# Optimization experiments

Measured on AMD Instinct MI355X. Metric: run time of the kernel, lower is better.

Reference implementation:

```python
import jax, jax.numpy as jnp
import numpy as np
import math

NUM_BLOCKS, NUM_LAYERS = 3, 10
CLASSES, RES_CH, DIL_CH, SKIP_CH, END_CH = 256, 32, 32, 256, 256
KERNEL = 2
OUTPUT_LENGTH = 32


def _dilation_schedule():
    sched = []
    init_d = 1
    for _ in range(NUM_BLOCKS):
        new_d = 1
        for _ in range(NUM_LAYERS):
            sched.append((new_d, init_d))
            init_d = new_d
            new_d *= 2
    return sched


def dilate(x, dilation, init_dilation):
    # pytorch-wavenet 'dilate': folds time into batch (or back) via reshape.
    if dilation == init_dilation:
        return x
    n, c, l = x.shape
    df = dilation / init_dilation
    new_l = int(math.ceil(l / df) * df)
    if new_l != l:
        x = jnp.pad(x, ((0, 0), (0, 0), (new_l - l, 0)))  # pad_start with zeros
        l = new_l
    l_new = int(round(l * init_dilation / dilation))
    n_new = int(round(n * dilation / init_dilation))
    # (n,c,l) -> (c,l,n) -> (c,l_new,n_new) -> (n_new,c,l_new)
    return x.transpose(1, 2, 0).reshape(c, l_new, n_new).transpose(2, 0, 1)


def conv1(x, w, b):  # 1x1 conv; w: (out,in)
    return jnp.einsum('oc,bcl->bol', w, x) + b[None, :, None]


def conv2(x, w, b):  # kernel-size-2 'valid' conv; w: (out,in,2)
    return (jnp.einsum('oc,bcl->bol', w[:, :, 0], x[:, :, :-1])
            + jnp.einsum('oc,bcl->bol', w[:, :, 1], x[:, :, 1:])
            + b[None, :, None])


def setup_inputs() -> dict:
    key = jax.random.key(0)
    ks = jax.random.split(key, 16)
    L = NUM_BLOCKS * NUM_LAYERS
    f32 = jnp.float32
    s_in = 1.0 / math.sqrt(CLASSES)
    s_res = 1.0 / math.sqrt(RES_CH * KERNEL)
    s_dil = 1.0 / math.sqrt(DIL_CH)
    s_skip = 1.0 / math.sqrt(SKIP_CH)
    return {
        'x': jax.random.normal(ks[0], (16, CLASSES, 4096), f32),
        'causal_w': jax.random.normal(ks[1], (RES_CH, CLASSES), f32) * s_in,
        'causal_b': jnp.zeros((RES_CH,), f32),
        'filt_w': jax.random.normal(ks[2], (L, DIL_CH, RES_CH, KERNEL), f32) * s_res,
        'filt_b': jnp.zeros((L, DIL_CH), f32),
        'gate_w': jax.random.normal(ks[3], (L, DIL_CH, RES_CH, KERNEL), f32) * s_res,
        'gate_b': jnp.zeros((L, DIL_CH), f32),
        'res_w': jax.random.normal(ks[4], (L, RES_CH, DIL_CH), f32) * s_dil,
        'res_b': jnp.zeros((L, RES_CH), f32),
        'skip_w': jax.random.normal(ks[5], (L, SKIP_CH, DIL_CH), f32) * s_dil,
        'skip_b': jnp.zeros((L, SKIP_CH), f32),
        'end1_w': jax.random.normal(ks[6], (END_CH, SKIP_CH), f32) * s_skip,
        'end1_b': jnp.zeros((END_CH,), f32),
        'end2_w': jax.random.normal(ks[7], (CLASSES, END_CH), f32) * (1.0 / math.sqrt(END_CH)),
        'end2_b': jnp.zeros((CLASSES,), f32),
    }


def reference(x, causal_w, causal_b, filt_w, filt_b, gate_w, gate_b,
              res_w, res_b, skip_w, skip_b, end1_w, end1_b, end2_w, end2_b):
    sched = _dilation_schedule()
    cur = conv1(x, causal_w, causal_b)  # (B, RES_CH, L)
    skip = None
    for i, (d, idil) in enumerate(sched):
        residual = dilate(cur, d, idil)
        f = jnp.tanh(conv2(residual, filt_w[i], filt_b[i]))
        g = jax.nn.sigmoid(conv2(residual, gate_w[i], gate_b[i]))
        z = f * g
        s = z if z.shape[2] == 1 else dilate(z, 1, d)
        s = conv1(s, skip_w[i], skip_b[i])
        skip = s if skip is None else s + skip[:, :, -s.shape[2]:]
        cur = conv1(z, res_w[i], res_b[i]) + residual[:, :, KERNEL - 1:]
    out = jax.nn.relu(skip)
    out = jax.nn.relu(conv1(out, end1_w, end1_b))
    out = conv1(out, end2_w, end2_b)
    n, c, _ = out.shape
    out = out[:, :, -OUTPUT_LENGTH:]
    return out.transpose(0, 2, 1).reshape(n * OUTPUT_LENGTH, c)
```

## Files before the change

kernel.cpp:

```cpp
#include <hip/hip_runtime.h>

#define BATCH   16
#define CLASSES 256
#define TLEN    4096
#define RC      32
#define SKIPC   256
#define ENDC    256
#define NLAYERS 30
#define OUT_T   32


__global__ __launch_bounds__(256) void causal_kernel(
    const float* __restrict__ x, const float* __restrict__ w,
    const float* __restrict__ bias, float* __restrict__ h0)
{
    const int NT = 97;
    int b    = blockIdx.x / NT;
    int tile = blockIdx.x % NT;
    int t0   = 995 + tile * 32;

    __shared__ float xs[CLASSES][32];
    __shared__ float wsm[CLASSES][33];

    for (int idx = threadIdx.x; idx < CLASSES * 32; idx += 256) {
        int cc = idx >> 5, j = idx & 31;
        int t = t0 + j;
        xs[cc][j] = (t < TLEN) ? x[((size_t)b * CLASSES + cc) * TLEN + t] : 0.0f;
    }
    for (int idx = threadIdx.x; idx < RC * CLASSES; idx += 256) {
        int c = idx >> 8, cc = idx & 255;
        wsm[cc][c] = w[idx];
    }
    __syncthreads();

    int c  = threadIdx.x & 31;
    int jb = threadIdx.x >> 5;
    float acc0 = 0.f, acc1 = 0.f, acc2 = 0.f, acc3 = 0.f;
    for (int cc = 0; cc < CLASSES; ++cc) {
        float wv = wsm[cc][c];
        const float4* xr = (const float4*)&xs[cc][0];
        float4 xv = xr[jb];
        acc0 += wv * xv.x; acc1 += wv * xv.y;
        acc2 += wv * xv.z; acc3 += wv * xv.w;
    }
    float bb = bias[c];
    float accs[4] = {acc0, acc1, acc2, acc3};
    #pragma unroll
    for (int k = 0; k < 4; ++k) {
        int t = t0 + jb * 4 + k;
        if (t < TLEN) h0[((size_t)b * RC + c) * TLEN + t] = accs[k] + bb;
    }
}

__global__ __launch_bounds__(256) void layer_kernel(
    const float* __restrict__ hin, float* __restrict__ hout,
    float* __restrict__ zb,
    const float* __restrict__ filt_w, const float* __restrict__ filt_b,
    const float* __restrict__ gate_w, const float* __restrict__ gate_b,
    const float* __restrict__ res_w,  const float* __restrict__ res_b,
    int layer, int d, int A1, int nTiles)
{
    int tile = blockIdx.x % nTiles;
    int b    = blockIdx.x / nTiles;
    int t_lo = 4032 - 64 * tile;

    __shared__ float hc[RC][68];
    __shared__ float hp[RC][68];
    __shared__ float zt[RC][68];
    __shared__ float wf0[RC][33], wf1[RC][33];
    __shared__ float wg0[RC][33], wg1[RC][33];
    __shared__ float wrs[RC][33];
    __shared__ float bfs[RC], bgs[RC], brs[RC];

    {
        const float* fw = filt_w + (size_t)layer * RC * RC * 2;
        const float* gw = gate_w + (size_t)layer * RC * RC * 2;
        const float* rw = res_w  + (size_t)layer * RC * RC;
        for (int idx = threadIdx.x; idx < RC * RC; idx += 256) {
            int c = idx >> 5, c2 = idx & 31;
            wf0[c][c2] = fw[idx * 2];  wf1[c][c2] = fw[idx * 2 + 1];
            wg0[c][c2] = gw[idx * 2];  wg1[c][c2] = gw[idx * 2 + 1];
            wrs[c][c2] = rw[idx];
        }
        if (threadIdx.x < RC) {
            bfs[threadIdx.x] = filt_b[layer * RC + threadIdx.x];
            bgs[threadIdx.x] = gate_b[layer * RC + threadIdx.x];
            brs[threadIdx.x] = res_b[layer * RC + threadIdx.x];
        }
    }
    for (int idx = threadIdx.x; idx < RC * 64; idx += 256) {
        int c2 = idx >> 6, tx = idx & 63;
        const float* row = hin + ((size_t)b * RC + c2) * TLEN;
        int t = t_lo + tx;
        hc[c2][tx] = row[t];
        hp[c2][tx] = row[t - d];
    }
    __syncthreads();

    int c  = threadIdx.x & 31;
    int tl = threadIdx.x >> 5;
    float fa[8], ga[8];
    float bfv = bfs[c], bgv = bgs[c];
    #pragma unroll
    for (int k = 0; k < 8; ++k) { fa[k] = bfv; ga[k] = bgv; }

    #pragma unroll 4
    for (int c2 = 0; c2 < RC; ++c2) {
        float w0f = wf0[c][c2], w1f = wf1[c][c2];
        float w0g = wg0[c][c2], w1g = wg1[c][c2];
        const float4* hcr = (const float4*)&hc[c2][0];
        const float4* hpr = (const float4*)&hp[c2][0];
        float4 c0 = hcr[tl * 2], c1 = hcr[tl * 2 + 1];
        float4 p0 = hpr[tl * 2], p1 = hpr[tl * 2 + 1];
        float hcv[8] = {c0.x, c0.y, c0.z, c0.w, c1.x, c1.y, c1.z, c1.w};
        float hpv[8] = {p0.x, p0.y, p0.z, p0.w, p1.x, p1.y, p1.z, p1.w};
        #pragma unroll
        for (int k = 0; k < 8; ++k) {
            fa[k] += w0f * hpv[k] + w1f * hcv[k];
            ga[k] += w0g * hpv[k] + w1g * hcv[k];
        }
    }
    #pragma unroll
    for (int k = 0; k < 8; ++k) {
        float e2 = __expf(2.0f * fa[k]);
        float th = 1.0f - 2.0f / (e2 + 1.0f);
        float sg = 1.0f / (1.0f + __expf(-ga[k]));
        zt[c][tl * 8 + k] = th * sg;
    }
    __syncthreads();

    float ra[8];
    float brv = brs[c];
    #pragma unroll
    for (int k = 0; k < 8; ++k) ra[k] = brv;
    #pragma unroll 4
    for (int c2 = 0; c2 < RC; ++c2) {
        float wv = wrs[c][c2];
        const float4* zr = (const float4*)&zt[c2][0];
        float4 z0 = zr[tl * 2], z1 = zr[tl * 2 + 1];
        float zv[8] = {z0.x, z0.y, z0.z, z0.w, z1.x, z1.y, z1.z, z1.w};
        #pragma unroll
        for (int k = 0; k < 8; ++k) ra[k] += wv * zv[k];
    }
    #pragma unroll
    for (int k = 0; k < 8; ++k) {
        int tx = tl * 8 + k;
        hp[c][tx] = hc[c][tx] + ra[k];
    }
    __syncthreads();

    for (int idx = threadIdx.x; idx < RC * 64; idx += 256) {
        int c2 = idx >> 6, tx = idx & 63;
        int t = t_lo + tx;
        if (t >= A1) hout[((size_t)b * RC + c2) * TLEN + t] = hp[c2][tx];
    }
    if (tile == 0) {
        for (int idx = threadIdx.x; idx < RC * OUT_T; idx += 256) {
            int c2 = idx >> 5, tt = idx & 31;
            zb[(((size_t)layer * BATCH + b) * RC + c2) * OUT_T + tt] = zt[c2][32 + tt];
        }
    }
}

__global__ __launch_bounds__(256) void end_kernel(
    const float* __restrict__ zb,
    const float* __restrict__ skip_w, const float* __restrict__ skip_b,
    const float* __restrict__ e1w, const float* __restrict__ e1b,
    const float* __restrict__ e2w, const float* __restrict__ e2b,
    float* __restrict__ out)
{
    int b  = blockIdx.x >> 5;
    int tt = blockIdx.x & 31;

    __shared__ float zv[NLAYERS * RC];
    __shared__ float sv[SKIPC];
    __shared__ float e1[ENDC];

    for (int idx = threadIdx.x; idx < NLAYERS * RC; idx += 256) {
        int i = idx >> 5, c = idx & 31;
        zv[idx] = zb[(((size_t)i * BATCH + b) * RC + c) * OUT_T + tt];
    }
    __syncthreads();

    int sc = threadIdx.x;
    float acc = 0.0f;
    for (int i = 0; i < NLAYERS; ++i) {
        acc += skip_b[i * SKIPC + sc];
        const float* sw = skip_w + ((size_t)i * SKIPC + sc) * RC;
        #pragma unroll 8
        for (int c2 = 0; c2 < RC; ++c2) acc += sw[c2] * zv[i * RC + c2];
    }
    sv[sc] = fmaxf(acc, 0.0f);
    __syncthreads();

    float a1 = e1b[sc];
    const float* w1 = e1w + (size_t)sc * SKIPC;
    #pragma unroll 8
    for (int k = 0; k < SKIPC; ++k) a1 += w1[k] * sv[k];
    e1[sc] = fmaxf(a1, 0.0f);
    __syncthreads();

    float a2 = e2b[sc];
    const float* w2 = e2w + (size_t)sc * ENDC;
    #pragma unroll 8
    for (int k = 0; k < ENDC; ++k) a2 += w2[k] * e1[k];
    out[(size_t)blockIdx.x * CLASSES + sc] = a2;
}

extern "C" void kernel_launch(void* const* d_in, const int* in_sizes, int n_in,
                              void* d_out, int out_size, void* d_ws, size_t ws_size,
                              hipStream_t stream)
{
    const float* x        = (const float*)d_in[0];
    const float* causal_w = (const float*)d_in[1];
    const float* causal_b = (const float*)d_in[2];
    const float* filt_w   = (const float*)d_in[3];
    const float* filt_b   = (const float*)d_in[4];
    const float* gate_w   = (const float*)d_in[5];
    const float* gate_b   = (const float*)d_in[6];
    const float* res_w    = (const float*)d_in[7];
    const float* res_b    = (const float*)d_in[8];
    const float* skip_w   = (const float*)d_in[9];
    const float* skip_b   = (const float*)d_in[10];
    const float* e1w      = (const float*)d_in[11];
    const float* e1b      = (const float*)d_in[12];
    const float* e2w      = (const float*)d_in[13];
    const float* e2b      = (const float*)d_in[14];

    const size_t HSZ = (size_t)BATCH * RC * TLEN;
    float* hA = (float*)d_ws;
    float* hB = hA + HSZ;
    float* zb = hB + HSZ;

    causal_kernel<<<dim3(BATCH * 97), dim3(256), 0, stream>>>(x, causal_w, causal_b, hA);

    float* bufs[2] = {hA, hB};
    int S = 3069;
    for (int i = 0; i < NLAYERS; ++i) {
        int d = 1 << (i % 10);
        S -= d;
        int A1    = 4064 - S;
        int nOut  = 4096 - A1;
        int nTiles = (nOut + 63) / 64;
        const float* hin = bufs[i & 1];
        float*       ho  = bufs[(i & 1) ^ 1];
        layer_kernel<<<dim3(BATCH * nTiles), dim3(256), 0, stream>>>(
            hin, ho, zb, filt_w, filt_b, gate_w, gate_b, res_w, res_b,
            i, d, A1, nTiles);
    }

    end_kernel<<<dim3(BATCH * OUT_T), dim3(256), 0, stream>>>(
        zb, skip_w, skip_b, e1w, e1b, e2w, e2b, (float*)d_out);
}
```

Measured before the change: 748.6 us.

## Replace per-column end kernel with three tiled GEMM kernels over all outputs

The single end kernel, which ran one block per (batch, time) column and re-read every weight from global memory in each block, is split into three shared-memory tiled GEMMs: skip accumulation, end1 and end2. Each block now handles a 32x32 tile of channels by columns, and the z buffer layout is changed to channel-major so the 512 columns can be batched together. This cuts redundant weight traffic from global memory. In exchange it adds two extra launches and global round trips for the intermediate activations, and each GEMM runs only 128 blocks.

```diff
diff --git a/kernel.cpp b/kernel.cpp
--- a/kernel.cpp
+++ b/kernel.cpp
@@ -8,6 +8,7 @@
 #define ENDC    256
 #define NLAYERS 30
 #define OUT_T   32
+#define NCOL    (BATCH * OUT_T)
 
 
 __global__ __launch_bounds__(256) void causal_kernel(
@@ -157,54 +158,144 @@
     if (tile == 0) {
         for (int idx = threadIdx.x; idx < RC * OUT_T; idx += 256) {
             int c2 = idx >> 5, tt = idx & 31;
-            zb[(((size_t)layer * BATCH + b) * RC + c2) * OUT_T + tt] = zt[c2][32 + tt];
-        }
-    }
-}
-
-__global__ __launch_bounds__(256) void end_kernel(
-    const float* __restrict__ zb,
+            zb[((size_t)layer * RC + c2) * NCOL + b * OUT_T + tt] = zt[c2][32 + tt];
+        }
+    }
+}
+
+__global__ __launch_bounds__(256) void skip_gemm_kernel(
     const float* __restrict__ skip_w, const float* __restrict__ skip_b,
-    const float* __restrict__ e1w, const float* __restrict__ e1b,
-    const float* __restrict__ e2w, const float* __restrict__ e2b,
-    float* __restrict__ out)
-{
-    int b  = blockIdx.x >> 5;
-    int tt = blockIdx.x & 31;
-
-    __shared__ float zv[NLAYERS * RC];
-    __shared__ float sv[SKIPC];
-    __shared__ float e1[ENDC];
-
-    for (int idx = threadIdx.x; idx < NLAYERS * RC; idx += 256) {
-        int i = idx >> 5, c = idx & 31;
-        zv[idx] = zb[(((size_t)i * BATCH + b) * RC + c) * OUT_T + tt];
-    }
-    __syncthreads();
-
-    int sc = threadIdx.x;
-    float acc = 0.0f;
+    const float* __restrict__ zb, float* __restrict__ skipv)
+{
+    int sc0 = blockIdx.x * 32;
+    int n0  = blockIdx.y * 32;
+
+    __shared__ float Ws[32][36];
+    __shared__ float Zs[32][36];
+    __shared__ float sbs[32];
+
+    if (threadIdx.x < 32) {
+        float s = 0.f;
+        #pragma unroll
+        for (int i = 0; i < NLAYERS; ++i) s += skip_b[i * SKIPC + sc0 + threadIdx.x];
+        sbs[threadIdx.x] = s;
+    }
+
+    int g = threadIdx.x >> 5;
+    int n = threadIdx.x & 31;
+    float acc[4] = {0.f, 0.f, 0.f, 0.f};
+
     for (int i = 0; i < NLAYERS; ++i) {
-        acc += skip_b[i * SKIPC + sc];
-        const float* sw = skip_w + ((size_t)i * SKIPC + sc) * RC;
-        #pragma unroll 8
-        for (int c2 = 0; c2 < RC; ++c2) acc += sw[c2] * zv[i * RC + c2];
-    }
-    sv[sc] = fmaxf(acc, 0.0f);
-    __syncthreads();
-
-    float a1 = e1b[sc];
-    const float* w1 = e1w + (size_t)sc * SKIPC;
-    #pragma unroll 8
-    for (int k = 0; k < SKIPC; ++k) a1 += w1[k] * sv[k];
-    e1[sc] = fmaxf(a1, 0.0f);
-    __syncthreads();
-
-    float a2 = e2b[sc];
-    const float* w2 = e2w + (size_t)sc * ENDC;
-    #pragma unroll 8
-    for (int k = 0; k < ENDC; ++k) a2 += w2[k] * e1[k];
-    out[(size_t)blockIdx.x * CLASSES + sc] = a2;
+        __syncthreads();
+        for (int idx = threadIdx.x; idx < 1024; idx += 256) {
+            int r = idx >> 5, cc = idx & 31;
+            Ws[r][cc] = skip_w[((size_t)i * SKIPC + sc0 + r) * RC + cc];
+        }
+        for (int idx = threadIdx.x; idx < 1024; idx += 256) {
+            int cc = idx >> 5, nn = idx & 31;
+            Zs[nn][cc] = zb[((size_t)i * RC + cc) * NCOL + n0 + nn];
+        }
+        __syncthreads();
+        #pragma unroll
+        for (int k4 = 0; k4 < 8; ++k4) {
+            float4 z4 = *(const float4*)&Zs[n][k4 * 4];
+            #pragma unroll
+            for (int q = 0; q < 4; ++q) {
+                float4 w4 = *(const float4*)&Ws[g + 8 * q][k4 * 4];
+                acc[q] += w4.x * z4.x + w4.y * z4.y + w4.z * z4.z + w4.w * z4.w;
+            }
+        }
+    }
+    #pragma unroll
+    for (int q = 0; q < 4; ++q) {
+        int sc = sc0 + g + 8 * q;
+        skipv[(size_t)sc * NCOL + n0 + n] = fmaxf(acc[q] + sbs[g + 8 * q], 0.f);
+    }
+}
+
+__global__ __launch_bounds__(256) void mid_gemm_kernel(
+    const float* __restrict__ A, const float* __restrict__ bias,
+    const float* __restrict__ V, float* __restrict__ O)
+{
+    int sc0 = blockIdx.x * 32;
+    int n0  = blockIdx.y * 32;
+    __shared__ float Ws[32][36];
+    __shared__ float Zs[32][36];
+
+    int g = threadIdx.x >> 5;
+    int n = threadIdx.x & 31;
+    float acc[4] = {0.f, 0.f, 0.f, 0.f};
+
+    for (int k0 = 0; k0 < SKIPC; k0 += 32) {
+        __syncthreads();
+        for (int idx = threadIdx.x; idx < 1024; idx += 256) {
+            int r = idx >> 5, cc = idx & 31;
+            Ws[r][cc] = A[(size_t)(sc0 + r) * SKIPC + k0 + cc];
+        }
+        for (int idx = threadIdx.x; idx < 1024; idx += 256) {
+            int cc = idx >> 5, nn = idx & 31;
+            Zs[nn][cc] = V[(size_t)(k0 + cc) * NCOL + n0 + nn];
+        }
+        __syncthreads();
+        #pragma unroll
+        for (int k4 = 0; k4 < 8; ++k4) {
+            float4 z4 = *(const float4*)&Zs[n][k4 * 4];
+            #pragma unroll
+            for (int q = 0; q < 4; ++q) {
+                float4 w4 = *(const float4*)&Ws[g + 8 * q][k4 * 4];
+                acc[q] += w4.x * z4.x + w4.y * z4.y + w4.z * z4.z + w4.w * z4.w;
+            }
+        }
+    }
+    #pragma unroll
+    for (int q = 0; q < 4; ++q) {
+        int sc = sc0 + g + 8 * q;
+        O[(size_t)sc * NCOL + n0 + n] = fmaxf(acc[q] + bias[sc], 0.f);
+    }
+}
+
+__global__ __launch_bounds__(256) void out_gemm_kernel(
+    const float* __restrict__ A, const float* __restrict__ bias,
+    const float* __restrict__ V, float* __restrict__ O)
+{
+    int sc0 = blockIdx.x * 32;
+    int n0  = blockIdx.y * 32;
+    __shared__ float Ws[32][36];
+    __shared__ float Zs[32][36];
+    __shared__ float Ot[32][33];
+
+    int g = threadIdx.x >> 5;
+    int n = threadIdx.x & 31;
+    float acc[4] = {0.f, 0.f, 0.f, 0.f};
+
+    for (int k0 = 0; k0 < ENDC; k0 += 32) {
+        __syncthreads();
+        for (int idx = threadIdx.x; idx < 1024; idx += 256) {
+            int r = idx >> 5, cc = idx & 31;
+            Ws[r][cc] = A[(size_t)(sc0 + r) * ENDC + k0 + cc];
+        }
+        for (int idx = threadIdx.x; idx < 1024; idx += 256) {
+            int cc = idx >> 5, nn = idx & 31;
+            Zs[nn][cc] = V[(size_t)(k0 + cc) * NCOL + n0 + nn];
+        }
+        __syncthreads();
+        #pragma unroll
+        for (int k4 = 0; k4 < 8; ++k4) {
+            float4 z4 = *(const float4*)&Zs[n][k4 * 4];
+            #pragma unroll
+            for (int q = 0; q < 4; ++q) {
+                float4 w4 = *(const float4*)&Ws[g + 8 * q][k4 * 4];
+                acc[q] += w4.x * z4.x + w4.y * z4.y + w4.z * z4.z + w4.w * z4.w;
+            }
+        }
+    }
+    #pragma unroll
+    for (int q = 0; q < 4; ++q) Ot[n][g + 8 * q] = acc[q] + bias[sc0 + g + 8 * q];
+    __syncthreads();
+    for (int idx = threadIdx.x; idx < 1024; idx += 256) {
+        int r = idx >> 5, cc = idx & 31;
+        O[(size_t)(n0 + r) * CLASSES + sc0 + cc] = Ot[r][cc];
+    }
 }
 
 extern "C" void kernel_launch(void* const* d_in, const int* in_sizes, int n_in,
@@ -228,9 +319,11 @@
     const float* e2b      = (const float*)d_in[14];
 
     const size_t HSZ = (size_t)BATCH * RC * TLEN;
-    float* hA = (float*)d_ws;
-    float* hB = hA + HSZ;
-    float* zb = hB + HSZ;
+    float* hA    = (float*)d_ws;
+    float* hB    = hA + HSZ;
+    float* zb    = hB + HSZ;
+    float* skipv = zb + (size_t)NLAYERS * RC * NCOL;
+    float* e1v   = skipv + (size_t)SKIPC * NCOL;
 
     causal_kernel<<<dim3(BATCH * 97), dim3(256), 0, stream>>>(x, causal_w, causal_b, hA);
 
@@ -239,8 +332,8 @@
     for (int i = 0; i < NLAYERS; ++i) {
         int d = 1 << (i % 10);
         S -= d;
-        int A1    = 4064 - S;
-        int nOut  = 4096 - A1;
+        int A1     = 4064 - S;
+        int nOut   = 4096 - A1;
         int nTiles = (nOut + 63) / 64;
         const float* hin = bufs[i & 1];
         float*       ho  = bufs[(i & 1) ^ 1];
@@ -249,6 +342,7 @@
             i, d, A1, nTiles);
     }
 
-    end_kernel<<<dim3(BATCH * OUT_T), dim3(256), 0, stream>>>(
-        zb, skip_w, skip_b, e1w, e1b, e2w, e2b, (float*)d_out);
-}
+    skip_gemm_kernel<<<dim3(8, 16), dim3(256), 0, stream>>>(skip_w, skip_b, zb, skipv);
+    mid_gemm_kernel <<<dim3(8, 16), dim3(256), 0, stream>>>(e1w, e1b, skipv, e1v);
+    out_gemm_kernel <<<dim3(8, 16), dim3(256), 0, stream>>>(e2w, e2b, e1v, (float*)d_out);
+}
```

New measurement: 802.8 us. 7.2% more time.

## Fuse layer chain and end MLP into one cooperative kernel with per-batch barriers

Applied to the files above, without the earlier changes.

Replaces the 30 per-layer launches and the end kernel with a single cooperative persistent kernel. Each batch element gets a group of 16 blocks that loop over time tiles and synchronise through atomic counters in global memory between layers. The skip, end1 and end2 stages are spread across the 16 blocks of each group, using shared-memory tiling with a reworked zb layout. This removes per-launch overhead and tail idle time, but adds spin-wait barriers, limits the grid to 256 blocks, and reloads weights once per layer in every block.

```diff
diff --git a/kernel.cpp b/kernel.cpp
--- a/kernel.cpp
+++ b/kernel.cpp
@@ -8,7 +8,9 @@
 #define ENDC    256
 #define NLAYERS 30
 #define OUT_T   32
-
+#define NCOL    512
+#define GBLK    16
+#define NBLK    256
 
 __global__ __launch_bounds__(256) void causal_kernel(
     const float* __restrict__ x, const float* __restrict__ w,
@@ -52,159 +54,244 @@
     }
 }
 
-__global__ __launch_bounds__(256) void layer_kernel(
-    const float* __restrict__ hin, float* __restrict__ hout,
-    float* __restrict__ zb,
+__device__ __forceinline__ void grp_barrier(unsigned* ctr)
+{
+    __syncthreads();
+    if (threadIdx.x == 0) {
+        __threadfence();
+        __hip_atomic_fetch_add(ctr, 1u, __ATOMIC_ACQ_REL, __HIP_MEMORY_SCOPE_AGENT);
+        while (__hip_atomic_load(ctr, __ATOMIC_ACQUIRE, __HIP_MEMORY_SCOPE_AGENT) < GBLK) {
+            __builtin_amdgcn_s_sleep(1);
+        }
+        __threadfence();
+    }
+    __syncthreads();
+}
+
+__global__ void __launch_bounds__(256) chain_kernel(
+    float* __restrict__ hA, float* __restrict__ hB,
+    float* __restrict__ zb, float* __restrict__ skipv, float* __restrict__ e1v,
+    unsigned* __restrict__ bar,
     const float* __restrict__ filt_w, const float* __restrict__ filt_b,
     const float* __restrict__ gate_w, const float* __restrict__ gate_b,
     const float* __restrict__ res_w,  const float* __restrict__ res_b,
-    int layer, int d, int A1, int nTiles)
-{
-    int tile = blockIdx.x % nTiles;
-    int b    = blockIdx.x / nTiles;
-    int t_lo = 4032 - 64 * tile;
-
-    __shared__ float hc[RC][68];
-    __shared__ float hp[RC][68];
-    __shared__ float zt[RC][68];
-    __shared__ float wf0[RC][33], wf1[RC][33];
-    __shared__ float wg0[RC][33], wg1[RC][33];
-    __shared__ float wrs[RC][33];
-    __shared__ float bfs[RC], bgs[RC], brs[RC];
-
-    {
-        const float* fw = filt_w + (size_t)layer * RC * RC * 2;
-        const float* gw = gate_w + (size_t)layer * RC * RC * 2;
-        const float* rw = res_w  + (size_t)layer * RC * RC;
-        for (int idx = threadIdx.x; idx < RC * RC; idx += 256) {
-            int c = idx >> 5, c2 = idx & 31;
-            wf0[c][c2] = fw[idx * 2];  wf1[c][c2] = fw[idx * 2 + 1];
-            wg0[c][c2] = gw[idx * 2];  wg1[c][c2] = gw[idx * 2 + 1];
-            wrs[c][c2] = rw[idx];
-        }
-        if (threadIdx.x < RC) {
-            bfs[threadIdx.x] = filt_b[layer * RC + threadIdx.x];
-            bgs[threadIdx.x] = gate_b[layer * RC + threadIdx.x];
-            brs[threadIdx.x] = res_b[layer * RC + threadIdx.x];
-        }
-    }
-    for (int idx = threadIdx.x; idx < RC * 64; idx += 256) {
-        int c2 = idx >> 6, tx = idx & 63;
-        const float* row = hin + ((size_t)b * RC + c2) * TLEN;
-        int t = t_lo + tx;
-        hc[c2][tx] = row[t];
-        hp[c2][tx] = row[t - d];
-    }
-    __syncthreads();
-
-    int c  = threadIdx.x & 31;
-    int tl = threadIdx.x >> 5;
-    float fa[8], ga[8];
-    float bfv = bfs[c], bgv = bgs[c];
-    #pragma unroll
-    for (int k = 0; k < 8; ++k) { fa[k] = bfv; ga[k] = bgv; }
-
-    #pragma unroll 4
-    for (int c2 = 0; c2 < RC; ++c2) {
-        float w0f = wf0[c][c2], w1f = wf1[c][c2];
-        float w0g = wg0[c][c2], w1g = wg1[c][c2];
-        const float4* hcr = (const float4*)&hc[c2][0];
-        const float4* hpr = (const float4*)&hp[c2][0];
-        float4 c0 = hcr[tl * 2], c1 = hcr[tl * 2 + 1];
-        float4 p0 = hpr[tl * 2], p1 = hpr[tl * 2 + 1];
-        float hcv[8] = {c0.x, c0.y, c0.z, c0.w, c1.x, c1.y, c1.z, c1.w};
-        float hpv[8] = {p0.x, p0.y, p0.z, p0.w, p1.x, p1.y, p1.z, p1.w};
-        #pragma unroll
-        for (int k = 0; k < 8; ++k) {
-            fa[k] += w0f * hpv[k] + w1f * hcv[k];
-            ga[k] += w0g * hpv[k] + w1g * hcv[k];
-        }
-    }
-    #pragma unroll
-    for (int k = 0; k < 8; ++k) {
-        float e2 = __expf(2.0f * fa[k]);
-        float th = 1.0f - 2.0f / (e2 + 1.0f);
-        float sg = 1.0f / (1.0f + __expf(-ga[k]));
-        zt[c][tl * 8 + k] = th * sg;
-    }
-    __syncthreads();
-
-    float ra[8];
-    float brv = brs[c];
-    #pragma unroll
-    for (int k = 0; k < 8; ++k) ra[k] = brv;
-    #pragma unroll 4
-    for (int c2 = 0; c2 < RC; ++c2) {
-        float wv = wrs[c][c2];
-        const float4* zr = (const float4*)&zt[c2][0];
-        float4 z0 = zr[tl * 2], z1 = zr[tl * 2 + 1];
-        float zv[8] = {z0.x, z0.y, z0.z, z0.w, z1.x, z1.y, z1.z, z1.w};
-        #pragma unroll
-        for (int k = 0; k < 8; ++k) ra[k] += wv * zv[k];
-    }
-    #pragma unroll
-    for (int k = 0; k < 8; ++k) {
-        int tx = tl * 8 + k;
-        hp[c][tx] = hc[c][tx] + ra[k];
-    }
-    __syncthreads();
-
-    for (int idx = threadIdx.x; idx < RC * 64; idx += 256) {
-        int c2 = idx >> 6, tx = idx & 63;
-        int t = t_lo + tx;
-        if (t >= A1) hout[((size_t)b * RC + c2) * TLEN + t] = hp[c2][tx];
-    }
-    if (tile == 0) {
-        for (int idx = threadIdx.x; idx < RC * OUT_T; idx += 256) {
-            int c2 = idx >> 5, tt = idx & 31;
-            zb[(((size_t)layer * BATCH + b) * RC + c2) * OUT_T + tt] = zt[c2][32 + tt];
-        }
-    }
-}
-
-__global__ __launch_bounds__(256) void end_kernel(
-    const float* __restrict__ zb,
     const float* __restrict__ skip_w, const float* __restrict__ skip_b,
     const float* __restrict__ e1w, const float* __restrict__ e1b,
     const float* __restrict__ e2w, const float* __restrict__ e2b,
     float* __restrict__ out)
 {
-    int b  = blockIdx.x >> 5;
-    int tt = blockIdx.x & 31;
-
-    __shared__ float zv[NLAYERS * RC];
-    __shared__ float sv[SKIPC];
-    __shared__ float e1[ENDC];
-
-    for (int idx = threadIdx.x; idx < NLAYERS * RC; idx += 256) {
-        int i = idx >> 5, c = idx & 31;
-        zv[idx] = zb[(((size_t)i * BATCH + b) * RC + c) * OUT_T + tt];
-    }
-    __syncthreads();
-
-    int sc = threadIdx.x;
-    float acc = 0.0f;
+    const int tid = threadIdx.x;
+    const int grp = blockIdx.x >> 4;
+    const int g   = blockIdx.x & 15;
+    const int b   = grp;
+
+    union __align__(16) Sh {
+        struct {
+            float hc[RC][68], hp[RC][68], zt[RC][68];
+            float wf0[RC][33], wf1[RC][33], wg0[RC][33], wg1[RC][33], wrs[RC][33];
+            float bfs[RC], bgs[RC], brs[RC];
+        } L;
+        struct { float z[320][32]; float w[10][16][32]; } E1;
+        struct { float v[256][32]; float w[16][256]; } E2;
+    };
+    __shared__ Sh sh;
+
+    int S = 3069;
     for (int i = 0; i < NLAYERS; ++i) {
-        acc += skip_b[i * SKIPC + sc];
-        const float* sw = skip_w + ((size_t)i * SKIPC + sc) * RC;
+        int d = 1 << (i % 10);
+        S -= d;
+        int A1 = 4064 - S;
+        int nT = (4096 - A1 + 63) >> 6;
+        const float* hin = (i & 1) ? hB : hA;
+        float*       hout = (i & 1) ? hA : hB;
+
+        if (g < nT) {
+            const float* fw = filt_w + (size_t)i * RC * RC * 2;
+            const float* gw = gate_w + (size_t)i * RC * RC * 2;
+            const float* rw = res_w  + (size_t)i * RC * RC;
+            for (int idx = tid; idx < RC * RC; idx += 256) {
+                int c = idx >> 5, c2 = idx & 31;
+                sh.L.wf0[c][c2] = fw[idx * 2];  sh.L.wf1[c][c2] = fw[idx * 2 + 1];
+                sh.L.wg0[c][c2] = gw[idx * 2];  sh.L.wg1[c][c2] = gw[idx * 2 + 1];
+                sh.L.wrs[c][c2] = rw[idx];
+            }
+            if (tid < RC) {
+                sh.L.bfs[tid] = filt_b[i * RC + tid];
+                sh.L.bgs[tid] = gate_b[i * RC + tid];
+                sh.L.brs[tid] = res_b[i * RC + tid];
+            }
+
+            for (int tile = g; tile < nT; tile += GBLK) {
+                int t_lo = 4032 - (tile << 6);
+                __syncthreads();
+                for (int idx = tid; idx < RC * 64; idx += 256) {
+                    int c2 = idx >> 6, tx = idx & 63;
+                    const float* row = hin + ((size_t)b * RC + c2) * TLEN;
+                    int t = t_lo + tx;
+                    sh.L.hc[c2][tx] = row[t];
+                    sh.L.hp[c2][tx] = row[t - d];
+                }
+                __syncthreads();
+
+                int c  = tid & 31;
+                int tl = tid >> 5;
+                float fa[8], ga[8];
+                float bfv = sh.L.bfs[c], bgv = sh.L.bgs[c];
+                #pragma unroll
+                for (int k = 0; k < 8; ++k) { fa[k] = bfv; ga[k] = bgv; }
+
+                #pragma unroll 4
+                for (int c2 = 0; c2 < RC; ++c2) {
+                    float w0f = sh.L.wf0[c][c2], w1f = sh.L.wf1[c][c2];
+                    float w0g = sh.L.wg0[c][c2], w1g = sh.L.wg1[c][c2];
+                    const float4* hcr = (const float4*)&sh.L.hc[c2][0];
+                    const float4* hpr = (const float4*)&sh.L.hp[c2][0];
+                    float4 c0 = hcr[tl * 2], c1 = hcr[tl * 2 + 1];
+                    float4 p0 = hpr[tl * 2], p1 = hpr[tl * 2 + 1];
+                    float hcv[8] = {c0.x, c0.y, c0.z, c0.w, c1.x, c1.y, c1.z, c1.w};
+                    float hpv[8] = {p0.x, p0.y, p0.z, p0.w, p1.x, p1.y, p1.z, p1.w};
+                    #pragma unroll
+                    for (int k = 0; k < 8; ++k) {
+                        fa[k] += w0f * hpv[k] + w1f * hcv[k];
+                        ga[k] += w0g * hpv[k] + w1g * hcv[k];
+                    }
+                }
+                #pragma unroll
+                for (int k = 0; k < 8; ++k) {
+                    float e2 = __expf(2.0f * fa[k]);
+                    float th = 1.0f - 2.0f / (e2 + 1.0f);
+                    float sg = 1.0f / (1.0f + __expf(-ga[k]));
+                    sh.L.zt[c][tl * 8 + k] = th * sg;
+                }
+                __syncthreads();
+
+                float ra[8];
+                float brv = sh.L.brs[c];
+                #pragma unroll
+                for (int k = 0; k < 8; ++k) ra[k] = brv;
+                #pragma unroll 4
+                for (int c2 = 0; c2 < RC; ++c2) {
+                    float wv = sh.L.wrs[c][c2];
+                    const float4* zr = (const float4*)&sh.L.zt[c2][0];
+                    float4 z0 = zr[tl * 2], z1 = zr[tl * 2 + 1];
+                    float zv[8] = {z0.x, z0.y, z0.z, z0.w, z1.x, z1.y, z1.z, z1.w};
+                    #pragma unroll
+                    for (int k = 0; k < 8; ++k) ra[k] += wv * zv[k];
+                }
+                #pragma unroll
+                for (int k = 0; k < 8; ++k) {
+                    int tx = tl * 8 + k;
+                    sh.L.hp[c][tx] = sh.L.hc[c][tx] + ra[k];
+                }
+                __syncthreads();
+
+                for (int idx = tid; idx < RC * 64; idx += 256) {
+                    int c2 = idx >> 6, tx = idx & 63;
+                    int t = t_lo + tx;
+                    if (t >= A1) hout[((size_t)b * RC + c2) * TLEN + t] = sh.L.hp[c2][tx];
+                }
+                if (tile == 0) {
+                    for (int idx = tid; idx < RC * OUT_T; idx += 256) {
+                        int c2 = idx >> 5, tt = idx & 31;
+                        zb[((size_t)i * RC + c2) * NCOL + b * OUT_T + tt] =
+                            sh.L.zt[c2][32 + tt];
+                    }
+                }
+            }
+        }
+        grp_barrier(bar + i * GBLK + grp);
+    }
+
+    const int n   = tid & 31;
+    const int s8  = tid >> 5;
+    const int sc0 = g * 16;
+
+    {
+        float a0 = 0.f, a1 = 0.f;
+        const float4* zb4 = (const float4*)zb;
+        const float4* sw4 = (const float4*)skip_w;
+        for (int ch = 0; ch < 3; ++ch) {
+            __syncthreads();
+            for (int idx = tid; idx < 320 * 8; idx += 256) {
+                int kk = idx >> 3, k4 = idx & 7;
+                ((float4*)&sh.E1.z[kk][0])[k4] = zb4[(size_t)(ch * 320 + kk) * 128 + b * 8 + k4];
+            }
+            for (int idx = tid; idx < 10 * 16 * 8; idx += 256) {
+                int l = idx >> 7, rem = idx & 127, r = rem >> 3, k4 = rem & 7;
+                ((float4*)&sh.E1.w[l][r][0])[k4] =
+                    sw4[((size_t)(ch * 10 + l) * SKIPC + sc0 + r) * 8 + k4];
+            }
+            __syncthreads();
+            #pragma unroll
+            for (int l = 0; l < 10; ++l) {
+                #pragma unroll
+                for (int k = 0; k < 32; ++k) {
+                    float zv = sh.E1.z[l * 32 + k][n];
+                    a0 += sh.E1.w[l][s8][k]     * zv;
+                    a1 += sh.E1.w[l][s8 + 8][k] * zv;
+                }
+            }
+        }
+        float sb0 = 0.f, sb1 = 0.f;
+        for (int l = 0; l < NLAYERS; ++l) {
+            sb0 += skip_b[l * SKIPC + sc0 + s8];
+            sb1 += skip_b[l * SKIPC + sc0 + s8 + 8];
+        }
+        skipv[((size_t)b * SKIPC + sc0 + s8) * 32 + n]     = fmaxf(a0 + sb0, 0.f);
+        skipv[((size_t)b * SKIPC + sc0 + s8 + 8) * 32 + n] = fmaxf(a1 + sb1, 0.f);
+    }
+    grp_barrier(bar + NLAYERS * GBLK + grp);
+
+    {
+        for (int idx = tid; idx < 256 * 8; idx += 256) {
+            int r = idx >> 3, k4 = idx & 7;
+            ((float4*)&sh.E2.v[r][0])[k4] =
+                ((const float4*)skipv)[((size_t)b * SKIPC + r) * 8 + k4];
+        }
+        for (int idx = tid; idx < 16 * 64; idx += 256) {
+            int r = idx >> 6, k4 = idx & 63;
+            ((float4*)&sh.E2.w[r][0])[k4] = ((const float4*)e1w)[(size_t)(sc0 + r) * 64 + k4];
+        }
+        __syncthreads();
+        float a0 = e1b[sc0 + s8], a1 = e1b[sc0 + s8 + 8];
         #pragma unroll 8
-        for (int c2 = 0; c2 < RC; ++c2) acc += sw[c2] * zv[i * RC + c2];
-    }
-    sv[sc] = fmaxf(acc, 0.0f);
-    __syncthreads();
-
-    float a1 = e1b[sc];
-    const float* w1 = e1w + (size_t)sc * SKIPC;
-    #pragma unroll 8
-    for (int k = 0; k < SKIPC; ++k) a1 += w1[k] * sv[k];
-    e1[sc] = fmaxf(a1, 0.0f);
-    __syncthreads();
-
-    float a2 = e2b[sc];
-    const float* w2 = e2w + (size_t)sc * ENDC;
-    #pragma unroll 8
-    for (int k = 0; k < ENDC; ++k) a2 += w2[k] * e1[k];
-    out[(size_t)blockIdx.x * CLASSES + sc] = a2;
+        for (int k4 = 0; k4 < 64; ++k4) {
+            float4 w0 = ((const float4*)&sh.E2.w[s8][0])[k4];
+            float4 w1 = ((const float4*)&sh.E2.w[s8 + 8][0])[k4];
+            float v0 = sh.E2.v[k4 * 4 + 0][n], v1 = sh.E2.v[k4 * 4 + 1][n];
+            float v2 = sh.E2.v[k4 * 4 + 2][n], v3 = sh.E2.v[k4 * 4 + 3][n];
+            a0 += w0.x * v0 + w0.y * v1 + w0.z * v2 + w0.w * v3;
+            a1 += w1.x * v0 + w1.y * v1 + w1.z * v2 + w1.w * v3;
+        }
+        e1v[((size_t)b * ENDC + sc0 + s8) * 32 + n]     = fmaxf(a0, 0.f);
+        e1v[((size_t)b * ENDC + sc0 + s8 + 8) * 32 + n] = fmaxf(a1, 0.f);
+    }
+    grp_barrier(bar + (NLAYERS + 1) * GBLK + grp);
+
+    {
+        for (int idx = tid; idx < 256 * 8; idx += 256) {
+            int r = idx >> 3, k4 = idx & 7;
+            ((float4*)&sh.E2.v[r][0])[k4] =
+                ((const float4*)e1v)[((size_t)b * ENDC + r) * 8 + k4];
+        }
+        for (int idx = tid; idx < 16 * 64; idx += 256) {
+            int r = idx >> 6, k4 = idx & 63;
+            ((float4*)&sh.E2.w[r][0])[k4] = ((const float4*)e2w)[(size_t)(sc0 + r) * 64 + k4];
+        }
+        __syncthreads();
+        float a0 = e2b[sc0 + s8], a1 = e2b[sc0 + s8 + 8];
+        #pragma unroll 8
+        for (int k4 = 0; k4 < 64; ++k4) {
+            float4 w0 = ((const float4*)&sh.E2.w[s8][0])[k4];
+            float4 w1 = ((const float4*)&sh.E2.w[s8 + 8][0])[k4];
+            float v0 = sh.E2.v[k4 * 4 + 0][n], v1 = sh.E2.v[k4 * 4 + 1][n];
+            float v2 = sh.E2.v[k4 * 4 + 2][n], v3 = sh.E2.v[k4 * 4 + 3][n];
+            a0 += w0.x * v0 + w0.y * v1 + w0.z * v2 + w0.w * v3;
+            a1 += w1.x * v0 + w1.y * v1 + w1.z * v2 + w1.w * v3;
+        }
+        out[(size_t)(b * OUT_T + n) * CLASSES + sc0 + s8]     = a0;
+        out[(size_t)(b * OUT_T + n) * CLASSES + sc0 + s8 + 8] = a1;
+    }
 }
 
 extern "C" void kernel_launch(void* const* d_in, const int* in_sizes, int n_in,
@@ -226,29 +313,26 @@
     const float* e1b      = (const float*)d_in[12];
     const float* e2w      = (const float*)d_in[13];
     const float* e2b      = (const float*)d_in[14];
+    float* outp           = (float*)d_out;
 
     const size_t HSZ = (size_t)BATCH * RC * TLEN;
-    float* hA = (float*)d_ws;
-    float* hB = hA + HSZ;
-    float* zb = hB + HSZ;
+    float* hA    = (float*)d_ws;
+    float* hB    = hA + HSZ;
+    float* zb    = hB + HSZ;
+    float* skipv = zb + (size_t)NLAYERS * RC * NCOL;
+    float* e1v   = skipv + (size_t)SKIPC * NCOL;
+    unsigned* bar = (unsigned*)(e1v + (size_t)ENDC * NCOL);
+
+    hipMemsetAsync(bar, 0, (NLAYERS + 2) * GBLK * sizeof(unsigned), stream);
 
     causal_kernel<<<dim3(BATCH * 97), dim3(256), 0, stream>>>(x, causal_w, causal_b, hA);
 
-    float* bufs[2] = {hA, hB};
-    int S = 3069;
-    for (int i = 0; i < NLAYERS; ++i) {
-        int d = 1 << (i % 10);
-        S -= d;
-        int A1    = 4064 - S;
-        int nOut  = 4096 - A1;
-        int nTiles = (nOut + 63) / 64;
-        const float* hin = bufs[i & 1];
-        float*       ho  = bufs[(i & 1) ^ 1];
-        layer_kernel<<<dim3(BATCH * nTiles), dim3(256), 0, stream>>>(
-            hin, ho, zb, filt_w, filt_b, gate_w, gate_b, res_w, res_b,
-            i, d, A1, nTiles);
-    }
-
-    end_kernel<<<dim3(BATCH * OUT_T), dim3(256), 0, stream>>>(
-        zb, skip_w, skip_b, e1w, e1b, e2w, e2b, (float*)d_out);
+    void* args[] = {
+        (void*)&hA, (void*)&hB, (void*)&zb, (void*)&skipv, (void*)&e1v, (void*)&bar,
+        (void*)&filt_w, (void*)&filt_b, (void*)&gate_w, (void*)&gate_b,
+        (void*)&res_w, (void*)&res_b, (void*)&skip_w, (void*)&skip_b,
+        (void*)&e1w, (void*)&e1b, (void*)&e2w, (void*)&e2b, (void*)&outp
+    };
+    hipLaunchCooperativeKernel((const void*)chain_kernel, dim3(NBLK), dim3(256),
+                               args, 0, stream);
 }
```

Measured after the change: 1.608 ms. +114.8%, slower.
